# Kernel optimization log

Measured on AMD Instinct MI355X. Metric: run time of the kernel, lower is better.

Reference implementation:

```python
import jax, jax.numpy as jnp
import numpy as np


def _conv2d_same(x, w):
    # x: [B,Cin,H,W], w: [Cout,Cin,3,3], stride 1, padding 1
    return jax.lax.conv_general_dilated(
        x, w, window_strides=(1, 1), padding=[(1, 1), (1, 1)],
        dimension_numbers=('NCHW', 'OIHW', 'NCHW'))


def _unfold3x3(x):
    # torch.nn.Unfold(kernel_size=3, padding=1, stride=1):
    # output [B, C*9, H*W], channel-major then kernel row-major ordering.
    b, c, h, w = x.shape
    xp = jnp.pad(x, ((0, 0), (0, 0), (1, 1), (1, 1)))
    patches = jnp.stack(
        [xp[:, :, i:i + h, j:j + w] for i in range(3) for j in range(3)],
        axis=2)  # [B, C, 9, H, W]
    return patches.reshape(b, c * 9, h * w)


def setup_inputs() -> dict:
    key = jax.random.key(0)
    ks = jax.random.split(key, 6)
    B, C, H, W = 16, 64, 128, 128
    R = 16
    return {
        'x': jax.random.normal(ks[0], (B, C, H, W), dtype=jnp.float32),
        'weight': jax.random.normal(ks[1], (C, C, 3, 3), dtype=jnp.float32) * 0.1,
        'se_w1': jax.random.normal(ks[2], (16, C, 3, 3), dtype=jnp.float32) * 0.1,
        'se_w2': jax.random.normal(ks[3], (1, 16, 3, 3), dtype=jnp.float32) * 0.1,
        'fc_w1': jax.random.normal(ks[4], (C // R, C), dtype=jnp.float32) * 0.1,
        'fc_w2': jax.random.normal(ks[5], (9 * C, C // R), dtype=jnp.float32) * 0.1,
    }


def reference(x, weight, se_w1, se_w2, fc_w1, fc_w2):
    b, c, h, w = x.shape
    # channel attention: global avg pool -> fc -> sigmoid, y: [B, C*9]
    y = x.mean(axis=(2, 3))                                   # [B, C]
    y = jax.nn.relu(y @ fc_w1.T)                              # [B, C//r]
    y = jax.nn.sigmoid(y @ fc_w2.T)                           # [B, 9C]
    # spatial attention A: [B, 1, H, W]
    A = jax.nn.sigmoid(_conv2d_same(jax.nn.relu(_conv2d_same(x, se_w1)), se_w2))
    out_unfold = _unfold3x3(x)                                # [B, C*9, HW]
    out_unfold = out_unfold * A.reshape(b, 1, h * w) * y[:, :, None]
    wf = weight.reshape(c, c * 9)                             # [Cout, C*9]
    out = jnp.einsum('bkl,ok->bol', out_unfold, wf)           # [B, Cout, HW]
    return out.reshape(b, c, h, w)
```

## Files before the change

### kernel.cpp

```cpp
#include <hip/hip_runtime.h>
#include <hip/hip_bf16.h>
#include <math.h>

#define B_  16
#define C_  64
#define H_  128
#define W_  128
#define HW_ (H_ * W_)
#define CR_ 4
#define K9C (9 * C_)
#define TW  130
#define FBS 36
#define STG_W 36
#define STG_H 12
#define MIDOFF (STG_H * STG_W * 128)
#define MIDS 18
#define WTB 8192
#define W2OFF (MIDOFF + 3 * WTB)
#define LDSZ  (W2OFF + 144 * 4)

typedef float f32x4 __attribute__((ext_vector_type(4)));
typedef __bf16 bf16x8 __attribute__((ext_vector_type(8)));

static __device__ __forceinline__ unsigned short f2us(float f) {
    __bf16 h = (__bf16)f;
    return __builtin_bit_cast(unsigned short, h);
}

static __device__ __forceinline__ int swz64(int blk) {
    int xcd = blk & 7, i = blk >> 3;
    return ((i >> 6) << 9) + (xcd << 6) + (i & 63);
}

__global__ void k_tr(const float* __restrict__ x, unsigned short* __restrict__ t,
                     float* __restrict__ y0) {
    int blk = blockIdx.x;
    int b = blk >> 7, y = blk & 127;
    __shared__ unsigned short lds[C_ * TW];
    int tid = threadIdx.x;
    for (int i = tid; i < C_ * 32; i += 256) {
        int c = i >> 5, xq = i & 31;
        float4 v = *(const float4*)(x + (((size_t)(b * C_ + c)) << 14) + (y << 7) + (xq << 2));
        unsigned int p0 = f2us(v.x) | ((unsigned int)f2us(v.y) << 16);
        unsigned int p1 = f2us(v.z) | ((unsigned int)f2us(v.w) << 16);
        *(unsigned int*)&lds[c * TW + (xq << 2)]     = p0;
        *(unsigned int*)&lds[c * TW + (xq << 2) + 2] = p1;
        float s4 = v.x + v.y + v.z + v.w;
        s4 += __shfl_down(s4, 16, 32);
        s4 += __shfl_down(s4, 8, 32);
        s4 += __shfl_down(s4, 4, 32);
        s4 += __shfl_down(s4, 2, 32);
        s4 += __shfl_down(s4, 1, 32);
        if ((tid & 31) == 0) atomicAdd(&y0[b * C_ + c], s4);
    }
    __syncthreads();
    size_t rowbase = ((size_t)(b * TW + y + 1)) * TW * C_;
    for (int j = tid; j < 128 * 16; j += 256) {
        int px = j >> 4, g = j & 15;
        unsigned short a0 = lds[(4 * g + 0) * TW + px];
        unsigned short a1 = lds[(4 * g + 1) * TW + px];
        unsigned short a2 = lds[(4 * g + 2) * TW + px];
        unsigned short a3 = lds[(4 * g + 3) * TW + px];
        uint2 wv;
        wv.x = a0 | ((unsigned int)a1 << 16);
        wv.y = a2 | ((unsigned int)a3 << 16);
        *(uint2*)(t + rowbase + (size_t)(px + 1) * C_ + (g << 2)) = wv;
    }
    if (tid < 16) {
        int px = (tid < 8) ? 0 : (TW - 1);
        int ch = tid & 7;
        uint4 z = {0, 0, 0, 0};
        *(uint4*)(t + rowbase + (size_t)px * C_ + ch * 8) = z;
    }
    if (y == 0) {
        size_t base = (size_t)b * TW * TW * C_;
        uint4 z = {0, 0, 0, 0};
        for (int i = tid; i < TW * C_ / 8; i += 256)
            *(uint4*)(t + base + (size_t)i * 8) = z;
    }
    if (y == 127) {
        size_t base = ((size_t)(b * TW + TW - 1)) * TW * C_;
        uint4 z = {0, 0, 0, 0};
        for (int i = tid; i < TW * C_ / 8; i += 256)
            *(uint4*)(t + base + (size_t)i * 8) = z;
    }
}

__global__ void k_attwt(const float* __restrict__ y0,
                        const float* __restrict__ fc_w1,
                        const float* __restrict__ fc_w2,
                        const float* __restrict__ weight,
                        const float* __restrict__ se_w1,
                        unsigned short* __restrict__ w_t,
                        unsigned short* __restrict__ w1t) {
    int blk = blockIdx.x;
    int b = blk >> 2, mt = blk & 3;
    __shared__ float sy0[C_];
    __shared__ float sh[CR_];
    __shared__ float ssy[K9C];
    __shared__ float sw[16 * 576];
    int tid = threadIdx.x;
    if (blk == 0) {
        for (int i = tid; i < 9 * 16 * C_; i += 256) {
            int tap = i >> 10, o = (i >> 6) & 15, c = i & 63;
            w1t[i] = f2us(se_w1[(o * C_ + c) * 9 + tap]);
        }
    }
    if (tid < C_) sy0[tid] = y0[b * C_ + tid] * (1.0f / (float)HW_);
    const float* wsrc = weight + (size_t)(mt * 16) * 576;
    for (int i = tid; i < 16 * 576; i += 256) sw[i] = wsrc[i];
    __syncthreads();
    if (tid < CR_) {
        float s = 0.f;
        for (int c = 0; c < C_; ++c) s = fmaf(fc_w1[tid * C_ + c], sy0[c], s);
        sh[tid] = fmaxf(s, 0.f);
    }
    __syncthreads();
    for (int i = tid; i < K9C; i += 256) {
        float s = 0.f;
        #pragma unroll
        for (int j = 0; j < CR_; ++j) s = fmaf(fc_w2[i * CR_ + j], sh[j], s);
        ssy[i] = 1.f / (1.f + expf(-s));
    }
    __syncthreads();
    unsigned short* wb = w_t + (size_t)b * 9 * C_ * C_;
    for (int ii = tid; ii < 4608; ii += 256) {
        int i = ii << 1;
        int tap = i >> 10, r = i & 1023;
        int half = r >> 9, lane = (r >> 3) & 63, e = r & 7;
        int o = lane & 15;
        int c = half * 32 + ((lane >> 4) << 3) + e;
        float v0 = sw[o * 576 + c * 9 + tap] * ssy[c * 9 + tap];
        float v1 = sw[o * 576 + (c + 1) * 9 + tap] * ssy[(c + 1) * 9 + tap];
        unsigned int pk = f2us(v0) | ((unsigned int)f2us(v1) << 16);
        *(unsigned int*)(wb + ((tap * 4 + mt) * 2 + half) * 512 + lane * 8 + e) = pk;
    }
}

__global__ void __launch_bounds__(512, 4)
k_fused(const unsigned short* __restrict__ t, const unsigned short* __restrict__ w_t,
        const unsigned short* __restrict__ w1t, const float* __restrict__ se_w2,
        float* __restrict__ out) {
    int blk = swz64(blockIdx.x);
    int b = blk >> 6, tile = blk & 63;
    int ty0 = (tile >> 2) << 3, tx0 = (tile & 3) << 5;
    int tid = threadIdx.x, lane = tid & 63, wave = tid >> 6;
    int wy = wave >> 1, wx = wave & 1;
    int n = lane & 15, q = lane >> 4, qc = q << 3;
    __shared__ __align__(16) char smem[LDSZ];
    float* fb  = (float*)smem;
    float* mid = (float*)(smem + MIDOFF);
    float* w2l = (float*)(smem + W2OFF);

    const unsigned short* tbb = t + (size_t)b * TW * TW * C_;
    for (int i = tid; i < STG_H * STG_W * 8; i += 512) {
        int row = i / (STG_W * 8), r = i % (STG_W * 8), px = r >> 3, ch = r & 7;
        int tr = ty0 - 1 + row; tr = tr < 0 ? 0 : (tr > TW - 1 ? TW - 1 : tr);
        int tc = tx0 - 1 + px;  tc = tc < 0 ? 0 : (tc > TW - 1 ? TW - 1 : tc);
        uint4 v = *(const uint4*)(tbb + ((size_t)tr * TW + tc) * C_ + ch * 8);
        *(uint4*)(smem + (row * STG_W + px) * 128 + ((ch ^ (px & 7)) << 4)) = v;
    }
    if (tid < 144) w2l[tid] = se_w2[(tid & 15) * 9 + (tid >> 4)];

    const unsigned short* wb = w_t + (size_t)b * 9 * C_ * C_;
    #define STAGE_WT(tp) \
        __builtin_amdgcn_global_load_lds( \
            (const __attribute__((address_space(1))) void*)(wb + (tp) * 4096 + (wave << 9) + (lane << 3)), \
            (__attribute__((address_space(3))) void*)(smem + MIDOFF + ((tp) % 3) * WTB + (wave << 10)), \
            16, 0, 0)
    STAGE_WT(0);
    STAGE_WT(1);
    __syncthreads();

    f32x4 acc[4][2] = {};
    #pragma unroll
    for (int tap = 0; tap < 9; ++tap) {
        if (tap) {
            if (tap < 8) asm volatile("s_waitcnt vmcnt(1)" ::: "memory");
            else         asm volatile("s_waitcnt vmcnt(0)" ::: "memory");
            __builtin_amdgcn_s_barrier();
            __builtin_amdgcn_sched_barrier(0);
        }
        if (tap < 7) STAGE_WT(tap + 2);
        int ki = tap / 3, kj = tap % 3;
        int xl = (wx << 4) + n + kj + 1;
        int xk = xl & 7;
        const char* tapbuf = smem + MIDOFF + (tap % 3) * WTB;
        __builtin_amdgcn_s_setprio(1);
        #pragma unroll
        for (int half = 0; half < 2; ++half) {
            bf16x8 af[4];
            #pragma unroll
            for (int mt = 0; mt < 4; ++mt) {
                uint4 au = *(const uint4*)(tapbuf + (((mt << 1) + half) << 10) + (lane << 4));
                af[mt] = __builtin_bit_cast(bf16x8, au);
            }
            int slot = (((half << 2) + q) ^ xk) << 4;
            #pragma unroll
            for (int j2 = 0; j2 < 2; ++j2) {
                int yl = (wy << 1) + j2 + ki + 1;
                bf16x8 bf = *(const bf16x8*)(smem + (yl * STG_W + xl) * 128 + slot);
                #pragma unroll
                for (int mt = 0; mt < 4; ++mt)
                    acc[mt][j2] = __builtin_amdgcn_mfma_f32_16x16x32_bf16(af[mt], bf, acc[mt][j2], 0, 0, 0);
            }
        }
        __builtin_amdgcn_s_setprio(0);
    }
    #undef STAGE_WT
    __syncthreads();

    int mr[3], mc[3], pp[3];
    bool on[3];
    #pragma unroll
    for (int i = 0; i < 3; ++i) {
        int g = wave + (i << 3);
        on[i] = (g < 22);
        int p = g * 16 + n; if (p > 339) p = 339;
        pp[i] = p; mr[i] = p / 34; mc[i] = p - mr[i] * 34;
    }
    f32x4 a1_0 = {}, a1_1 = {}, a1_2 = {};
    #pragma unroll
    for (int tap = 0; tap < 9; ++tap) {
        int ki = tap / 3, kj = tap % 3;
        uint4 u0 = *(const uint4*)(w1t + (tap * 16 + n) * C_ + qc);
        uint4 u1 = *(const uint4*)(w1t + (tap * 16 + n) * C_ + 32 + qc);
        bf16x8 af0 = __builtin_bit_cast(bf16x8, u0);
        bf16x8 af1 = __builtin_bit_cast(bf16x8, u1);
        #pragma unroll
        for (int i = 0; i < 3; ++i) {
            if (on[i]) {
                int sc = mc[i] + kj;
                int sb = ((mr[i] + ki) * STG_W + sc) * 128;
                bf16x8 b0 = *(const bf16x8*)(smem + sb + ((q ^ (sc & 7)) << 4));
                bf16x8 b1 = *(const bf16x8*)(smem + sb + (((4 + q) ^ (sc & 7)) << 4));
                f32x4 t0 = (i == 0) ? a1_0 : (i == 1) ? a1_1 : a1_2;
                t0 = __builtin_amdgcn_mfma_f32_16x16x32_bf16(af0, b0, t0, 0, 0, 0);
                t0 = __builtin_amdgcn_mfma_f32_16x16x32_bf16(af1, b1, t0, 0, 0, 0);
                if (i == 0) a1_0 = t0; else if (i == 1) a1_1 = t0; else a1_2 = t0;
            }
        }
    }
    #pragma unroll
    for (int i = 0; i < 3; ++i) {
        int g = wave + (i << 3);
        if (on[i] && (g < 21 || n < 4)) {
            int my = ty0 - 1 + mr[i], mx = tx0 - 1 + mc[i];
            bool valid = (my >= 0) && (my < 128) && (mx >= 0) && (mx < 128);
            f32x4 av = (i == 0) ? a1_0 : (i == 1) ? a1_1 : a1_2;
            #pragma unroll
            for (int r = 0; r < 4; ++r)
                mid[pp[i] * MIDS + (q << 2) + r] = valid ? fmaxf(av[r], 0.f) : 0.f;
        }
    }
    __syncthreads();

    float4 wq[9];
    #pragma unroll
    for (int tap = 0; tap < 9; ++tap)
        wq[tap] = *(const float4*)&w2l[tap * 16 + (q << 2)];
    float Av[2];
    #pragma unroll
    for (int j2 = 0; j2 < 2; ++j2) {
        float s = 0.f;
        #pragma unroll
        for (int di = 0; di < 3; ++di) {
            #pragma unroll
            for (int dj = 0; dj < 3; ++dj) {
                int p = ((wy << 1) + j2 + di) * 34 + (wx << 4) + n + dj;
                const float* mp = &mid[p * MIDS + (q << 2)];
                float2 m0 = *(const float2*)mp;
                float2 m1 = *(const float2*)(mp + 2);
                float4 wv = wq[di * 3 + dj];
                s = fmaf(m0.x, wv.x, s);
                s = fmaf(m0.y, wv.y, s);
                s = fmaf(m1.x, wv.z, s);
                s = fmaf(m1.y, wv.w, s);
            }
        }
        s += __shfl_xor(s, 16, 64);
        s += __shfl_xor(s, 32, 64);
        Av[j2] = 1.f / (1.f + expf(-s));
    }

    #pragma unroll
    for (int j2 = 0; j2 < 2; ++j2) {
        __syncthreads();
        #pragma unroll
        for (int mt = 0; mt < 4; ++mt) {
            #pragma unroll
            for (int r = 0; r < 4; ++r) {
                int o = (mt << 4) + (q << 2) + r;
                fb[((wy << 6) + o) * FBS + (wx << 4) + n] = acc[mt][j2][r] * Av[j2];
            }
        }
        __syncthreads();
        #pragma unroll
        for (int it = 0; it < 4; ++it) {
            int s = it * 512 + tid;
            int row = s >> 3, xq = s & 7;
            int wy2 = row >> 6, o = row & 63;
            float4 v = *(const float4*)&fb[row * FBS + (xq << 2)];
            *(float4*)(out + (((size_t)(b * C_ + o)) << 14) +
                       ((ty0 + (wy2 << 1) + j2) << 7) + tx0 + (xq << 2)) = v;
        }
    }
}

extern "C" void kernel_launch(void* const* d_in, const int* in_sizes, int n_in,
                              void* d_out, int out_size, void* d_ws, size_t ws_size,
                              hipStream_t stream) {
    const float* x      = (const float*)d_in[0];
    const float* weight = (const float*)d_in[1];
    const float* se_w1  = (const float*)d_in[2];
    const float* se_w2  = (const float*)d_in[3];
    const float* fc_w1  = (const float*)d_in[4];
    const float* fc_w2  = (const float*)d_in[5];
    float* out = (float*)d_out;

    char* ws = (char*)d_ws;
    float* y0            = (float*)ws;                         ws += 4096;
    unsigned short* t    = (unsigned short*)ws;                ws += (size_t)B_ * TW * TW * C_ * 2 + 4096;
    unsigned short* w_t  = (unsigned short*)ws;                ws += (size_t)B_ * 9 * C_ * C_ * 2;
    unsigned short* w1t  = (unsigned short*)ws;

    hipMemsetAsync(y0, 0, 4096, stream);
    k_tr   <<<B_ * H_, 256, 0, stream>>>(x, t, y0);
    k_attwt<<<B_ * 4, 256, 0, stream>>>(y0, fc_w1, fc_w2, weight, se_w1, w_t, w1t);
    k_fused<<<B_ * 64, 512, 0, stream>>>(t, w_t, w1t, se_w2, out);
}
```

Baseline: 193.4 us.

## Replace atomic pooling with partials, async LDS staging, single-pass output store

The global average pool now writes per-row partial sums and reduces them in the attention kernel, which removes the atomics and the memset launch. Input tile staging in the fused kernel uses global_load_lds direct-to-LDS copies with the swizzle applied on the source side rather than on the LDS address. The SE conv1 MFMA loop runs at raised wave priority. The output epilogue writes both row halves to LDS before a single barrier and then does one store pass, dropping two barriers at the cost of a larger fb footprint.

```diff
diff --git a/kernel.cpp b/kernel.cpp
--- a/kernel.cpp
+++ b/kernel.cpp
@@ -33,7 +33,7 @@
 }
 
 __global__ void k_tr(const float* __restrict__ x, unsigned short* __restrict__ t,
-                     float* __restrict__ y0) {
+                     float* __restrict__ y0p) {
     int blk = blockIdx.x;
     int b = blk >> 7, y = blk & 127;
     __shared__ unsigned short lds[C_ * TW];
@@ -51,7 +51,7 @@
         s4 += __shfl_down(s4, 4, 32);
         s4 += __shfl_down(s4, 2, 32);
         s4 += __shfl_down(s4, 1, 32);
-        if ((tid & 31) == 0) atomicAdd(&y0[b * C_ + c], s4);
+        if ((tid & 31) == 0) y0p[(((b << 7) + y) << 6) + c] = s4;
     }
     __syncthreads();
     size_t rowbase = ((size_t)(b * TW + y + 1)) * TW * C_;
@@ -86,7 +86,7 @@
     }
 }
 
-__global__ void k_attwt(const float* __restrict__ y0,
+__global__ void k_attwt(const float* __restrict__ y0p,
                         const float* __restrict__ fc_w1,
                         const float* __restrict__ fc_w2,
                         const float* __restrict__ weight,
@@ -106,7 +106,12 @@
             w1t[i] = f2us(se_w1[(o * C_ + c) * 9 + tap]);
         }
     }
-    if (tid < C_) sy0[tid] = y0[b * C_ + tid] * (1.0f / (float)HW_);
+    if (tid < C_) {
+        float s = 0.f;
+        const float* pp = y0p + ((size_t)b << 13) + tid;
+        for (int y = 0; y < 128; ++y) s += pp[y << 6];
+        sy0[tid] = s * (1.0f / (float)HW_);
+    }
     const float* wsrc = weight + (size_t)(mt * 16) * 576;
     for (int i = tid; i < 16 * 576; i += 256) sw[i] = wsrc[i];
     __syncthreads();
@@ -153,12 +158,18 @@
     float* w2l = (float*)(smem + W2OFF);
 
     const unsigned short* tbb = t + (size_t)b * TW * TW * C_;
-    for (int i = tid; i < STG_H * STG_W * 8; i += 512) {
-        int row = i / (STG_W * 8), r = i % (STG_W * 8), px = r >> 3, ch = r & 7;
-        int tr = ty0 - 1 + row; tr = tr < 0 ? 0 : (tr > TW - 1 ? TW - 1 : tr);
-        int tc = tx0 - 1 + px;  tc = tc < 0 ? 0 : (tc > TW - 1 ? TW - 1 : tc);
-        uint4 v = *(const uint4*)(tbb + ((size_t)tr * TW + tc) * C_ + ch * 8);
-        *(uint4*)(smem + (row * STG_W + px) * 128 + ((ch ^ (px & 7)) << 4)) = v;
+    #pragma unroll
+    for (int it = 0; it < 7; ++it) {
+        int s = (it << 9) + tid;
+        if (s < STG_H * STG_W * 8) {
+            int row = s / 288, r = s % 288, px = r >> 3, chp = r & 7;
+            int tr = ty0 - 1 + row; tr = tr < 0 ? 0 : (tr > TW - 1 ? TW - 1 : tr);
+            int tc = tx0 - 1 + px;  tc = tc < 0 ? 0 : (tc > TW - 1 ? TW - 1 : tc);
+            int ch = chp ^ (px & 7);
+            __builtin_amdgcn_global_load_lds(
+                (const __attribute__((address_space(1))) void*)(tbb + ((size_t)tr * TW + tc) * C_ + (ch << 3)),
+                (__attribute__((address_space(3))) void*)(smem + (s << 4)), 16, 0, 0);
+        }
     }
     if (tid < 144) w2l[tid] = se_w2[(tid & 15) * 9 + (tid >> 4)];
 
@@ -220,6 +231,7 @@
         pp[i] = p; mr[i] = p / 34; mc[i] = p - mr[i] * 34;
     }
     f32x4 a1_0 = {}, a1_1 = {}, a1_2 = {};
+    __builtin_amdgcn_s_setprio(1);
     #pragma unroll
     for (int tap = 0; tap < 9; ++tap) {
         int ki = tap / 3, kj = tap % 3;
@@ -241,6 +253,7 @@
             }
         }
     }
+    __builtin_amdgcn_s_setprio(0);
     #pragma unroll
     for (int i = 0; i < 3; ++i) {
         int g = wave + (i << 3);
@@ -283,27 +296,28 @@
         Av[j2] = 1.f / (1.f + expf(-s));
     }
 
+    __syncthreads();
     #pragma unroll
     for (int j2 = 0; j2 < 2; ++j2) {
-        __syncthreads();
         #pragma unroll
         for (int mt = 0; mt < 4; ++mt) {
             #pragma unroll
             for (int r = 0; r < 4; ++r) {
                 int o = (mt << 4) + (q << 2) + r;
-                fb[((wy << 6) + o) * FBS + (wx << 4) + n] = acc[mt][j2][r] * Av[j2];
-            }
-        }
-        __syncthreads();
-        #pragma unroll
-        for (int it = 0; it < 4; ++it) {
-            int s = it * 512 + tid;
-            int row = s >> 3, xq = s & 7;
-            int wy2 = row >> 6, o = row & 63;
-            float4 v = *(const float4*)&fb[row * FBS + (xq << 2)];
-            *(float4*)(out + (((size_t)(b * C_ + o)) << 14) +
-                       ((ty0 + (wy2 << 1) + j2) << 7) + tx0 + (xq << 2)) = v;
-        }
+                fb[((j2 << 8) + (wy << 6) + o) * FBS + (wx << 4) + n] = acc[mt][j2][r] * Av[j2];
+            }
+        }
+    }
+    __syncthreads();
+    #pragma unroll
+    for (int it = 0; it < 8; ++it) {
+        int s = it * 512 + tid;
+        int row = s >> 3, xq = s & 7;
+        int j2 = row >> 8, rr = row & 255;
+        int wy2 = rr >> 6, o = rr & 63;
+        float4 v = *(const float4*)&fb[row * FBS + (xq << 2)];
+        *(float4*)(out + (((size_t)(b * C_ + o)) << 14) +
+                   ((ty0 + (wy2 << 1) + j2) << 7) + tx0 + (xq << 2)) = v;
     }
 }
 
@@ -319,13 +333,12 @@
     float* out = (float*)d_out;
 
     char* ws = (char*)d_ws;
-    float* y0            = (float*)ws;                         ws += 4096;
+    float* y0p           = (float*)ws;                         ws += (size_t)B_ * H_ * C_ * 4;
     unsigned short* t    = (unsigned short*)ws;                ws += (size_t)B_ * TW * TW * C_ * 2 + 4096;
     unsigned short* w_t  = (unsigned short*)ws;                ws += (size_t)B_ * 9 * C_ * C_ * 2;
     unsigned short* w1t  = (unsigned short*)ws;
 
-    hipMemsetAsync(y0, 0, 4096, stream);
-    k_tr   <<<B_ * H_, 256, 0, stream>>>(x, t, y0);
-    k_attwt<<<B_ * 4, 256, 0, stream>>>(y0, fc_w1, fc_w2, weight, se_w1, w_t, w1t);
+    k_tr   <<<B_ * H_, 256, 0, stream>>>(x, t, y0p);
+    k_attwt<<<B_ * 4, 256, 0, stream>>>(y0p, fc_w1, fc_w2, weight, se_w1, w_t, w1t);
     k_fused<<<B_ * 64, 512, 0, stream>>>(t, w_t, w1t, se_w2, out);
 }
```

New measurement: 175.3 us. 9.4% less time.
